# Kernel tuning notes

Hardware: AMD Instinct MI355X
Metric: run time of the kernel (lower is better)

Reference implementation:

```python
import jax, jax.numpy as jnp
from jax import lax
import numpy as np

BALANCE = 1.0  # polynomial kernel: (conv(x,w)+b + BALANCE)**POWER
POWER = 2


def _conv(x, w, b, stride, pad):
    y = lax.conv_general_dilated(
        x, w, window_strides=(stride, stride),
        padding=[(pad, pad), (pad, pad)],
        dimension_numbers=('NCHW', 'OIHW', 'NCHW'))
    return y + b[None, :, None, None]


def kerv2d(x, w, b, stride, pad):
    # PolyKervNets degree-2 polynomial kervolution
    y = _conv(x, w, b, stride, pad) + BALANCE
    return y * y  # (.)**2


def avgpool3s2(x):
    s = lax.reduce_window(x, 0.0, lax.add, (1, 1, 3, 3), (1, 1, 2, 2), 'VALID')
    return s * (1.0 / 9.0)


def setup_inputs() -> dict:
    key = jax.random.key(0)
    ks = jax.random.split(key, 17)
    sc = 0.01  # small init so repeated squaring stays numerically sane
    d = {}
    d['x'] = jax.random.normal(ks[0], (64, 3, 227, 227), jnp.float32)
    d['w1'] = jax.random.normal(ks[1], (96, 3, 11, 11), jnp.float32) * sc
    d['b1'] = jnp.zeros((96,), jnp.float32)
    d['w2'] = jax.random.normal(ks[2], (256, 96, 5, 5), jnp.float32) * sc
    d['b2'] = jnp.zeros((256,), jnp.float32)
    d['w3'] = jax.random.normal(ks[3], (384, 256, 3, 3), jnp.float32) * sc
    d['b3'] = jnp.zeros((384,), jnp.float32)
    d['w4'] = jax.random.normal(ks[4], (384, 384, 3, 3), jnp.float32) * sc
    d['b4'] = jnp.zeros((384,), jnp.float32)
    d['w5'] = jax.random.normal(ks[5], (256, 384, 3, 3), jnp.float32) * sc
    d['b5'] = jnp.zeros((256,), jnp.float32)
    d['fw1'] = jax.random.normal(ks[6], (9216, 4096), jnp.float32) * sc
    d['fb1'] = jnp.zeros((4096,), jnp.float32)
    d['fw2'] = jax.random.normal(ks[7], (4096, 4096), jnp.float32) * sc
    d['fb2'] = jnp.zeros((4096,), jnp.float32)
    d['fw3'] = jax.random.normal(ks[8], (4096, 1000), jnp.float32) * sc
    d['fb3'] = jnp.zeros((1000,), jnp.float32)
    return d


def reference(x, w1, b1, w2, b2, w3, b3, w4, b4, w5, b5,
              fw1, fb1, fw2, fb2, fw3, fb3):
    x = kerv2d(x, w1, b1, stride=4, pad=0)   # [B,96,55,55]
    x = avgpool3s2(x)                        # [B,96,27,27]
    x = kerv2d(x, w2, b2, stride=1, pad=2)   # [B,256,27,27]
    x = avgpool3s2(x)                        # [B,256,13,13]
    x = kerv2d(x, w3, b3, stride=1, pad=1)   # [B,384,13,13]
    x = kerv2d(x, w4, b4, stride=1, pad=1)   # [B,384,13,13]
    x = kerv2d(x, w5, b5, stride=1, pad=1)   # [B,256,13,13]
    x = avgpool3s2(x)                        # [B,256,6,6]
    x = x.reshape(x.shape[0], -1)            # [B,9216]
    x = x @ fw1 + fb1
    x = x @ fw2 + fb2
    x = x @ fw3 + fb3
    return x
```

## Files before the change

### kernel.cpp

```cpp
#include <hip/hip_runtime.h>


typedef _Float16 f16;
typedef _Float16 f16x8 __attribute__((ext_vector_type(8)));
typedef float    f32x4 __attribute__((ext_vector_type(4)));

#define CDIV(a,b) (((a)+(b)-1)/(b))

template<int C,int H,int W,int OC,int R,int S,int PAD,int STRIDE,int OH,int OW,
         bool SCALARB,int BM,int BN>
__global__ __launch_bounds__(256)
void conv_mfma(const f16* __restrict__ in, const f16* __restrict__ wt,
               const float* __restrict__ bias, f16* __restrict__ out)
{
    constexpr int KTOT = C * R * S;
    constexpr int KP   = (KTOT + 31) & ~31;
    constexpr int OHW  = OH * OW;
    constexpr int NTOT = 64 * OHW;
    constexpr int AM   = BM / 32;
    constexpr int AN   = BN / 32;
    constexpr int AU   = BM * 4 / 256;
    constexpr int BU   = BN * 4 / 256;

    __shared__ __align__(16) f16 As[BM * 32];
    __shared__ __align__(16) f16 Bs[BN * 32];

    const int t   = threadIdx.x;
    const int n0  = blockIdx.x * BN;
    const int oc0 = blockIdx.y * BM;

    int a_row[AU], a_g[AU], a_lds[AU]; bool a_ok[AU];
    #pragma unroll
    for (int i = 0; i < AU; ++i) {
        const int u = t + i * 256;
        a_row[i] = u >> 2;
        a_g[i]   = u & 3;
        a_lds[i] = a_row[i] * 32 + ((a_g[i] ^ (a_row[i] & 3)) * 8);
        a_ok[i]  = (oc0 + a_row[i]) < OC;
    }
    int b_row[BU], b_g[BU], b_lds[BU], b_img[BU], b_oy[BU], b_ox[BU]; bool b_ok[BU];
    #pragma unroll
    for (int i = 0; i < BU; ++i) {
        const int u = t + i * 256;
        b_row[i] = u >> 2;
        b_g[i]   = u & 3;
        b_lds[i] = b_row[i] * 32 + ((b_g[i] ^ (b_row[i] & 3)) * 8);
        const int n   = n0 + b_row[i];
        b_ok[i]       = n < NTOT;
        const int ncl = b_ok[i] ? n : 0;
        b_img[i] = ncl / OHW;
        const int rem = ncl - b_img[i] * OHW;
        b_oy[i]  = rem / OW;
        b_ox[i]  = rem - b_oy[i] * OW;
    }

    const int wv = t >> 6;
    const int wm = (wv >> 1) * (BM / 2);
    const int wn = (wv & 1) * (BN / 2);
    const int l  = t & 63;
    const int il = l & 15;
    const int q  = l >> 4;

    f32x4 acc[AM][AN];
    #pragma unroll
    for (int i = 0; i < AM; ++i)
        #pragma unroll
        for (int j = 0; j < AN; ++j)
            acc[i][j] = (f32x4){0.f, 0.f, 0.f, 0.f};

    int4 aReg[AU], bReg[BU];

    auto loadA = [&](int kc) {
        #pragma unroll
        for (int i = 0; i < AU; ++i) {
            int4 v = {0, 0, 0, 0};
            if (a_ok[i])
                v = *(const int4*)(wt + (size_t)(oc0 + a_row[i]) * KP + kc + a_g[i] * 8);
            aReg[i] = v;
        }
    };
    auto loadB = [&](int kc) {
        #pragma unroll
        for (int i = 0; i < BU; ++i) {
            if (SCALARB) {
                const size_t sb = ((size_t)(b_img[i] * H + b_oy[i] * STRIDE) * W
                                   + b_ox[i] * STRIDE) * C;
                union { f16 h[8]; int4 v; } cv;
                #pragma unroll
                for (int j = 0; j < 8; ++j) {
                    const int k = kc + b_g[i] * 8 + j;
                    f16 v = (f16)0.f;
                    if (b_ok[i] && k < KTOT) {
                        const int r  = k / (S * C);
                        const int sc = k - r * (S * C);
                        v = in[sb + (size_t)r * (W * C) + sc];
                    }
                    cv.h[j] = v;
                }
                bReg[i] = cv.v;
            } else {
                const int k8 = kc + b_g[i] * 8;
                const int rs = k8 / C;
                const int c0 = k8 - rs * C;
                const int r  = rs / S;
                const int s  = rs - r * S;
                const int iy = b_oy[i] * STRIDE + r - PAD;
                const int ix = b_ox[i] * STRIDE + s - PAD;
                int4 v = {0, 0, 0, 0};
                if (b_ok[i] && iy >= 0 && iy < H && ix >= 0 && ix < W)
                    v = *(const int4*)(in + ((size_t)(b_img[i] * H + iy) * W + ix) * C + c0);
                bReg[i] = v;
            }
        }
    };

    loadA(0); loadB(0);

    for (int kc = 0; kc < KP; kc += 32) {
        #pragma unroll
        for (int i = 0; i < AU; ++i) *(int4*)&As[a_lds[i]] = aReg[i];
        #pragma unroll
        for (int i = 0; i < BU; ++i) *(int4*)&Bs[b_lds[i]] = bReg[i];
        __syncthreads();

        if (kc + 32 < KP) { loadA(kc + 32); loadB(kc + 32); }

        f16x8 af[AM], bf[AN];
        #pragma unroll
        for (int mi = 0; mi < AM; ++mi) {
            const int row = wm + mi * 16 + il;
            af[mi] = *(const f16x8*)&As[row * 32 + ((q ^ (row & 3)) * 8)];
        }
        #pragma unroll
        for (int ni = 0; ni < AN; ++ni) {
            const int row = wn + ni * 16 + il;
            bf[ni] = *(const f16x8*)&Bs[row * 32 + ((q ^ (row & 3)) * 8)];
        }
        #pragma unroll
        for (int mi = 0; mi < AM; ++mi)
            #pragma unroll
            for (int ni = 0; ni < AN; ++ni)
                acc[mi][ni] = __builtin_amdgcn_mfma_f32_16x16x32_f16(
                    af[mi], bf[ni], acc[mi][ni], 0, 0, 0);
        __syncthreads();
    }

    #pragma unroll
    for (int mi = 0; mi < AM; ++mi) {
        const int ocb = oc0 + wm + mi * 16 + q * 4;
        if (ocb >= OC) continue;
        const float4 bb = *(const float4*)(bias + ocb);
        const float b4[4] = {bb.x + 1.f, bb.y + 1.f, bb.z + 1.f, bb.w + 1.f};
        #pragma unroll
        for (int ni = 0; ni < AN; ++ni) {
            const int nn = n0 + wn + ni * 16 + il;
            if (nn >= NTOT) continue;
            const f32x4 v = acc[mi][ni];
            union { f16 h[4]; uint2 u; } cv;
            const float vv[4] = {v.x, v.y, v.z, v.w};
            #pragma unroll
            for (int rr = 0; rr < 4; ++rr) {
                const float y = vv[rr] + b4[rr];
                cv.h[rr] = (f16)(y * y);
            }
            *(uint2*)(out + (size_t)nn * OC + ocb) = cv.u;
        }
    }
}

template<bool TAIL>
__global__ __launch_bounds__(256)
void fc_mfma2(const f16* __restrict__ X, const float* __restrict__ Wm,
              float* __restrict__ P, int N, int Npad, int K, int kchunk)
{
    __shared__ __align__(16) f16 Xs[64 * 32];
    __shared__ __align__(16) f16 Ws[256 * 32];

    const int t  = threadIdx.x;
    const int n0 = blockIdx.x * 256;
    const int s  = blockIdx.y;
    const int k0 = s * kchunk;
    const int nIter = kchunk / 32;

    const bool wok = !TAIL || (n0 + t) < N;
    const float* __restrict__ wbase = Wm + (size_t)k0 * N + n0 + t;
    const int xm = t >> 2;
    const int xg = t & 3;
    const f16* __restrict__ xbase = X + (size_t)xm * K + k0 + xg * 8;
    const int xoff = xm * 32 + (xg ^ (xm & 3)) * 8;

    const int wq = t >> 6;
    const int l  = t & 63;
    const int il = l & 15;
    const int q  = l >> 4;

    f32x4 acc[4][4];
    #pragma unroll
    for (int i = 0; i < 4; ++i)
        #pragma unroll
        for (int j = 0; j < 4; ++j)
            acc[i][j] = (f32x4){0.f, 0.f, 0.f, 0.f};

    float wreg[4][8];
    int4  xreg;

    auto loadChunk = [&](int it) {
        const size_t kbase = (size_t)it * 32;
        #pragma unroll
        for (int g = 0; g < 4; ++g)
            #pragma unroll
            for (int j = 0; j < 8; ++j)
                wreg[g][j] = wok ? wbase[(kbase + g * 8 + j) * N] : 0.f;
        xreg = *(const int4*)(xbase + kbase);
    };

    loadChunk(0);

    for (int it = 0; it < nIter; ++it) {
        #pragma unroll
        for (int g = 0; g < 4; ++g) {
            f16x8 h;
            #pragma unroll
            for (int j = 0; j < 8; ++j) h[j] = (f16)wreg[g][j];
            *(f16x8*)&Ws[t * 32 + (g ^ (t & 3)) * 8] = h;
        }
        *(int4*)&Xs[xoff] = xreg;
        __syncthreads();

        if (it + 1 < nIter) loadChunk(it + 1);

        f16x8 af[4], bf[4];
        #pragma unroll
        for (int mi = 0; mi < 4; ++mi) {
            const int m = mi * 16 + il;
            af[mi] = *(const f16x8*)&Xs[m * 32 + (q ^ (m & 3)) * 8];
        }
        #pragma unroll
        for (int ni = 0; ni < 4; ++ni) {
            const int n = wq * 64 + ni * 16 + il;
            bf[ni] = *(const f16x8*)&Ws[n * 32 + (q ^ (n & 3)) * 8];
        }
        #pragma unroll
        for (int mi = 0; mi < 4; ++mi)
            #pragma unroll
            for (int ni = 0; ni < 4; ++ni)
                acc[mi][ni] = __builtin_amdgcn_mfma_f32_16x16x32_f16(
                    af[mi], bf[ni], acc[mi][ni], 0, 0, 0);
        __syncthreads();
    }

    float* __restrict__ pb = P + (size_t)s * 64 * Npad + n0;
    #pragma unroll
    for (int mi = 0; mi < 4; ++mi) {
        const int m = mi * 16 + q * 4;
        #pragma unroll
        for (int ni = 0; ni < 4; ++ni) {
            const int n = wq * 64 + ni * 16 + il;
            const f32x4 v = acc[mi][ni];
            const float vv[4] = {v.x, v.y, v.z, v.w};
            #pragma unroll
            for (int rr = 0; rr < 4; ++rr)
                pb[(size_t)(m + rr) * Npad + n] = vv[rr];
        }
    }
}

template<bool F16OUT>
__global__ __launch_bounds__(256)
void fc_reduce(const float* __restrict__ P, const float* __restrict__ bias,
               f16* __restrict__ o16, float* __restrict__ o32,
               int N, int Npad, int S)
{
    const int idx = blockIdx.x * 256 + threadIdx.x;
    const int total = 64 * (N / 4);
    if (idx >= total) return;
    const int n4 = (idx % (N / 4)) * 4;
    const int m  = idx / (N / 4);
    float4 a = *(const float4*)(bias + n4);
    const float* __restrict__ p = P + (size_t)m * Npad + n4;
    for (int s = 0; s < S; ++s) {
        const float4 v = *(const float4*)(p + (size_t)s * 64 * Npad);
        a.x += v.x; a.y += v.y; a.z += v.z; a.w += v.w;
    }
    if (F16OUT) {
        union { f16 h[4]; uint2 u; } cv;
        cv.h[0] = (f16)a.x; cv.h[1] = (f16)a.y;
        cv.h[2] = (f16)a.z; cv.h[3] = (f16)a.w;
        *(uint2*)(o16 + (size_t)m * N + n4) = cv.u;
    } else {
        *(float4*)(o32 + (size_t)m * N + n4) = a;
    }
}

__global__ __launch_bounds__(256)
void avgpool_nhwc(const f16* __restrict__ in, f16* __restrict__ out,
                  int C, int H, int W, int OH, int OW, int total)
{
    const int idx = blockIdx.x * 256 + threadIdx.x;
    if (idx >= total) return;
    const int c   = idx % C;
    int rest      = idx / C;
    const int ox  = rest % OW; rest /= OW;
    const int oy  = rest % OH;
    const int b   = rest / OH;
    const f16* __restrict__ p = in + ((size_t)(b * H + oy * 2) * W + ox * 2) * C + c;
    float s = 0.f;
    #pragma unroll
    for (int r = 0; r < 3; ++r)
        #pragma unroll
        for (int cc = 0; cc < 3; ++cc)
            s += (float)p[(r * W + cc) * C];
    out[idx] = (f16)(s * (1.f / 9.f));
}

__global__ __launch_bounds__(256)
void pool5_ncflat(const f16* __restrict__ in, f16* __restrict__ out)
{
    const int idx = blockIdx.x * 256 + threadIdx.x;
    if (idx >= 64 * 6 * 6 * 256) return;
    const int c  = idx & 255;
    int rest     = idx >> 8;
    const int ox = rest % 6; rest /= 6;
    const int oy = rest % 6;
    const int b  = rest / 6;
    const f16* __restrict__ p = in + ((size_t)(b * 13 + oy * 2) * 13 + ox * 2) * 256 + c;
    float s = 0.f;
    #pragma unroll
    for (int r = 0; r < 3; ++r)
        #pragma unroll
        for (int cc = 0; cc < 3; ++cc)
            s += (float)p[(r * 13 + cc) * 256];
    out[(size_t)b * 9216 + c * 36 + oy * 6 + ox] = (f16)(s * (1.f / 9.f));
}

__global__ __launch_bounds__(256)
void x_to_nhwc(const float* __restrict__ x, f16* __restrict__ o)
{
    const int idx = blockIdx.x * 256 + threadIdx.x;
    if (idx >= 64 * 227 * 227) return;
    const int hw = idx % (227 * 227);
    const int b  = idx / (227 * 227);
    const size_t plane = 227 * 227;
    const float* __restrict__ p = x + (size_t)b * 3 * plane + hw;
    f16* __restrict__ po = o + (size_t)idx * 3;
    po[0] = (f16)p[0];
    po[1] = (f16)p[plane];
    po[2] = (f16)p[2 * plane];
}

__global__ __launch_bounds__(256)
void wt_tf(const float* __restrict__ w, f16* __restrict__ o,
           int OC, int Cc, int R, int S, int KP)
{
    const int idx = blockIdx.x * 256 + threadIdx.x;
    if (idx >= OC * KP) return;
    const int k  = idx % KP;
    const int oc = idx / KP;
    f16 v = (f16)0.f;
    if (k < Cc * R * S) {
        const int rs = k / Cc;
        const int c  = k - rs * Cc;
        const int r  = rs / S;
        const int s  = rs - r * S;
        v = (f16)w[(((size_t)oc * Cc + c) * R + r) * S + s];
    }
    o[idx] = v;
}

extern "C" void kernel_launch(void* const* d_in, const int* in_sizes, int n_in,
                              void* d_out, int out_size, void* d_ws, size_t ws_size,
                              hipStream_t stream)
{
    const float* x   = (const float*)d_in[0];
    const float* w1  = (const float*)d_in[1];
    const float* b1  = (const float*)d_in[2];
    const float* w2  = (const float*)d_in[3];
    const float* b2  = (const float*)d_in[4];
    const float* w3  = (const float*)d_in[5];
    const float* b3  = (const float*)d_in[6];
    const float* w4  = (const float*)d_in[7];
    const float* b4  = (const float*)d_in[8];
    const float* w5  = (const float*)d_in[9];
    const float* b5  = (const float*)d_in[10];
    const float* fw1 = (const float*)d_in[11];
    const float* fb1 = (const float*)d_in[12];
    const float* fw2 = (const float*)d_in[13];
    const float* fb2 = (const float*)d_in[14];
    const float* fw3 = (const float*)d_in[15];
    const float* fb3 = (const float*)d_in[16];
    float* out = (float*)d_out;

    char* ws = (char*)d_ws;
    const size_t MiB = 1024 * 1024;

    f16*   X0  = (f16*)(ws);
    f16*   Xh1 = (f16*)(ws);
    f16*   Xh2 = (f16*)(ws + 2 * MiB);
    f16*   Xh3 = (f16*)(ws + 2 * MiB + 512 * 1024);
    float* P   = (float*)(ws + 3 * MiB);
    f16*   A   = (f16*)(ws + 20 * MiB);
    f16*   Bp  = (f16*)(ws + 58 * MiB);
    f16*   Wt1 = (f16*)(ws + 84 * MiB);
    f16*   Wt2 = Wt1 + (size_t)96  * 384;
    f16*   Wt3 = Wt2 + (size_t)256 * 2400;
    f16*   Wt4 = Wt3 + (size_t)384 * 2304;
    f16*   Wt5 = Wt4 + (size_t)384 * 3456;

    wt_tf<<<CDIV(96  * 384 , 256), 256, 0, stream>>>(w1, Wt1, 96 , 3  , 11, 11, 384);
    wt_tf<<<CDIV(256 * 2400, 256), 256, 0, stream>>>(w2, Wt2, 256, 96 , 5 , 5 , 2400);
    wt_tf<<<CDIV(384 * 2304, 256), 256, 0, stream>>>(w3, Wt3, 384, 256, 3 , 3 , 2304);
    wt_tf<<<CDIV(384 * 3456, 256), 256, 0, stream>>>(w4, Wt4, 384, 384, 3 , 3 , 3456);
    wt_tf<<<CDIV(256 * 3456, 256), 256, 0, stream>>>(w5, Wt5, 256, 384, 3 , 3 , 3456);

    x_to_nhwc<<<CDIV(64 * 227 * 227, 256), 256, 0, stream>>>(x, X0);

    conv_mfma<3,227,227,96,11,11,0,4,55,55,true,128,128>
        <<<dim3(CDIV(64 * 55 * 55, 128), 1), 256, 0, stream>>>(X0, Wt1, b1, A);
    {
        int total = 64 * 27 * 27 * 96;
        avgpool_nhwc<<<CDIV(total, 256), 256, 0, stream>>>(A, Bp, 96, 55, 55, 27, 27, total);
    }
    conv_mfma<96,27,27,256,5,5,2,1,27,27,false,128,128>
        <<<dim3(CDIV(64 * 27 * 27, 128), 2), 256, 0, stream>>>(Bp, Wt2, b2, A);
    {
        int total = 64 * 13 * 13 * 256;
        avgpool_nhwc<<<CDIV(total, 256), 256, 0, stream>>>(A, Bp, 256, 27, 27, 13, 13, total);
    }
    conv_mfma<256,13,13,384,3,3,1,1,13,13,false,128,64>
        <<<dim3(169, 3), 256, 0, stream>>>(Bp, Wt3, b3, A);
    conv_mfma<384,13,13,384,3,3,1,1,13,13,false,128,64>
        <<<dim3(169, 3), 256, 0, stream>>>(A, Wt4, b4, Bp);
    conv_mfma<384,13,13,256,3,3,1,1,13,13,false,128,64>
        <<<dim3(169, 2), 256, 0, stream>>>(Bp, Wt5, b5, A);

    pool5_ncflat<<<CDIV(64 * 6 * 6 * 256, 256), 256, 0, stream>>>(A, Xh1);

    fc_mfma2<false><<<dim3(16, 16), 256, 0, stream>>>(Xh1, fw1, P, 4096, 4096, 9216, 576);
    fc_reduce<true><<<CDIV(64 * 4096 / 4, 256), 256, 0, stream>>>(P, fb1, Xh2, nullptr, 4096, 4096, 16);
    fc_mfma2<false><<<dim3(16, 16), 256, 0, stream>>>(Xh2, fw2, P, 4096, 4096, 4096, 256);
    fc_reduce<true><<<CDIV(64 * 4096 / 4, 256), 256, 0, stream>>>(P, fb2, Xh3, nullptr, 4096, 4096, 16);
    fc_mfma2<true><<<dim3(4, 64), 256, 0, stream>>>(Xh3, fw3, P, 1000, 1024, 4096, 64);
    fc_reduce<false><<<CDIV(64 * 1000 / 4, 256), 256, 0, stream>>>(P, fb3, nullptr, out, 1000, 1024, 64);
}
```

Baseline: 718.9 us.

## Pad conv1 input to 4 channels for vectorized im2col and vectorize avgpool

Pads the input image to NHWC with 4 channels so each conv1 kernel row becomes a contiguous run of 48 halves (12 pixels by 4 channels). The B-tile gather can then use two 8-byte loads instead of eight scalar loads with index math, and the conv1 weights are repacked to match the padded layout. Average pooling is vectorized to process 8 channels per thread with 16-byte loads and stores. The LDS swizzle is changed to use row bits 2-3, and the workspace layout is reshuffled. The cost is a larger padded K for conv1 (544 vs 384), which adds MFMA work that is partly zeros.

```diff
diff --git a/kernel.cpp b/kernel.cpp
--- a/kernel.cpp
+++ b/kernel.cpp
@@ -6,14 +6,15 @@
 typedef float    f32x4 __attribute__((ext_vector_type(4)));
 
 #define CDIV(a,b) (((a)+(b)-1)/(b))
+#define SWZ(row,g) ((g) ^ (((row) >> 2) & 3))
 
 template<int C,int H,int W,int OC,int R,int S,int PAD,int STRIDE,int OH,int OW,
-         bool SCALARB,int BM,int BN>
+         int KRUN,int BM,int BN>
 __global__ __launch_bounds__(256)
 void conv_mfma(const f16* __restrict__ in, const f16* __restrict__ wt,
                const float* __restrict__ bias, f16* __restrict__ out)
 {
-    constexpr int KTOT = C * R * S;
+    constexpr int KTOT = (KRUN > 0) ? (R * KRUN) : (C * R * S);
     constexpr int KP   = (KTOT + 31) & ~31;
     constexpr int OHW  = OH * OW;
     constexpr int NTOT = 64 * OHW;
@@ -35,7 +36,7 @@
         const int u = t + i * 256;
         a_row[i] = u >> 2;
         a_g[i]   = u & 3;
-        a_lds[i] = a_row[i] * 32 + ((a_g[i] ^ (a_row[i] & 3)) * 8);
+        a_lds[i] = a_row[i] * 32 + SWZ(a_row[i], a_g[i]) * 8;
         a_ok[i]  = (oc0 + a_row[i]) < OC;
     }
     int b_row[BU], b_g[BU], b_lds[BU], b_img[BU], b_oy[BU], b_ox[BU]; bool b_ok[BU];
@@ -44,7 +45,7 @@
         const int u = t + i * 256;
         b_row[i] = u >> 2;
         b_g[i]   = u & 3;
-        b_lds[i] = b_row[i] * 32 + ((b_g[i] ^ (b_row[i] & 3)) * 8);
+        b_lds[i] = b_row[i] * 32 + SWZ(b_row[i], b_g[i]) * 8;
         const int n   = n0 + b_row[i];
         b_ok[i]       = n < NTOT;
         const int ncl = b_ok[i] ? n : 0;
@@ -82,22 +83,19 @@
     auto loadB = [&](int kc) {
         #pragma unroll
         for (int i = 0; i < BU; ++i) {
-            if (SCALARB) {
-                const size_t sb = ((size_t)(b_img[i] * H + b_oy[i] * STRIDE) * W
-                                   + b_ox[i] * STRIDE) * C;
-                union { f16 h[8]; int4 v; } cv;
-                #pragma unroll
-                for (int j = 0; j < 8; ++j) {
-                    const int k = kc + b_g[i] * 8 + j;
-                    f16 v = (f16)0.f;
-                    if (b_ok[i] && k < KTOT) {
-                        const int r  = k / (S * C);
-                        const int sc = k - r * (S * C);
-                        v = in[sb + (size_t)r * (W * C) + sc];
-                    }
-                    cv.h[j] = v;
+            if constexpr (KRUN > 0) {
+                const int k8 = kc + b_g[i] * 8;
+                const int r  = k8 / KRUN;
+                const int j0 = k8 - r * KRUN;
+                int4 v = {0, 0, 0, 0};
+                if (b_ok[i] && k8 < KTOT) {
+                    const f16* p = in + ((size_t)(b_img[i] * H + b_oy[i] * STRIDE + r) * W
+                                         + b_ox[i] * STRIDE) * C + j0;
+                    const int2 lo = *(const int2*)p;
+                    const int2 hi = *(const int2*)(p + 4);
+                    v.x = lo.x; v.y = lo.y; v.z = hi.x; v.w = hi.y;
                 }
-                bReg[i] = cv.v;
+                bReg[i] = v;
             } else {
                 const int k8 = kc + b_g[i] * 8;
                 const int rs = k8 / C;
@@ -129,12 +127,12 @@
         #pragma unroll
         for (int mi = 0; mi < AM; ++mi) {
             const int row = wm + mi * 16 + il;
-            af[mi] = *(const f16x8*)&As[row * 32 + ((q ^ (row & 3)) * 8)];
+            af[mi] = *(const f16x8*)&As[row * 32 + SWZ(row, q) * 8];
         }
         #pragma unroll
         for (int ni = 0; ni < AN; ++ni) {
             const int row = wn + ni * 16 + il;
-            bf[ni] = *(const f16x8*)&Bs[row * 32 + ((q ^ (row & 3)) * 8)];
+            bf[ni] = *(const f16x8*)&Bs[row * 32 + SWZ(row, q) * 8];
         }
         #pragma unroll
         for (int mi = 0; mi < AM; ++mi)
@@ -187,7 +185,7 @@
     const int xm = t >> 2;
     const int xg = t & 3;
     const f16* __restrict__ xbase = X + (size_t)xm * K + k0 + xg * 8;
-    const int xoff = xm * 32 + (xg ^ (xm & 3)) * 8;
+    const int xoff = xm * 32 + SWZ(xm, xg) * 8;
 
     const int wq = t >> 6;
     const int l  = t & 63;
@@ -222,7 +220,7 @@
             f16x8 h;
             #pragma unroll
             for (int j = 0; j < 8; ++j) h[j] = (f16)wreg[g][j];
-            *(f16x8*)&Ws[t * 32 + (g ^ (t & 3)) * 8] = h;
+            *(f16x8*)&Ws[t * 32 + SWZ(t, g) * 8] = h;
         }
         *(int4*)&Xs[xoff] = xreg;
         __syncthreads();
@@ -233,12 +231,12 @@
         #pragma unroll
         for (int mi = 0; mi < 4; ++mi) {
             const int m = mi * 16 + il;
-            af[mi] = *(const f16x8*)&Xs[m * 32 + (q ^ (m & 3)) * 8];
+            af[mi] = *(const f16x8*)&Xs[m * 32 + SWZ(m, q) * 8];
         }
         #pragma unroll
         for (int ni = 0; ni < 4; ++ni) {
             const int n = wq * 64 + ni * 16 + il;
-            bf[ni] = *(const f16x8*)&Ws[n * 32 + (q ^ (n & 3)) * 8];
+            bf[ni] = *(const f16x8*)&Ws[n * 32 + SWZ(n, q) * 8];
         }
         #pragma unroll
         for (int mi = 0; mi < 4; ++mi)
@@ -293,24 +291,30 @@
 }
 
 __global__ __launch_bounds__(256)
-void avgpool_nhwc(const f16* __restrict__ in, f16* __restrict__ out,
-                  int C, int H, int W, int OH, int OW, int total)
-{
-    const int idx = blockIdx.x * 256 + threadIdx.x;
-    if (idx >= total) return;
-    const int c   = idx % C;
-    int rest      = idx / C;
+void avgpool_nhwc8(const f16* __restrict__ in, f16* __restrict__ out,
+                   int C8, int C, int H, int W, int OH, int OW, int total8)
+{
+    const int idx = blockIdx.x * 256 + threadIdx.x;
+    if (idx >= total8) return;
+    const int c8  = (idx % C8) * 8;
+    int rest      = idx / C8;
     const int ox  = rest % OW; rest /= OW;
     const int oy  = rest % OH;
     const int b   = rest / OH;
-    const f16* __restrict__ p = in + ((size_t)(b * H + oy * 2) * W + ox * 2) * C + c;
-    float s = 0.f;
+    const f16* __restrict__ p = in + ((size_t)(b * H + oy * 2) * W + ox * 2) * C + c8;
+    float s[8] = {0.f, 0.f, 0.f, 0.f, 0.f, 0.f, 0.f, 0.f};
     #pragma unroll
     for (int r = 0; r < 3; ++r)
         #pragma unroll
-        for (int cc = 0; cc < 3; ++cc)
-            s += (float)p[(r * W + cc) * C];
-    out[idx] = (f16)(s * (1.f / 9.f));
+        for (int cc = 0; cc < 3; ++cc) {
+            const f16x8 v = *(const f16x8*)&p[(r * W + cc) * C];
+            #pragma unroll
+            for (int j = 0; j < 8; ++j) s[j] += (float)v[j];
+        }
+    f16x8 o8;
+    #pragma unroll
+    for (int j = 0; j < 8; ++j) o8[j] = (f16)(s[j] * (1.f / 9.f));
+    *(f16x8*)(out + (size_t)idx * 8) = o8;
 }
 
 __global__ __launch_bounds__(256)
@@ -334,7 +338,7 @@
 }
 
 __global__ __launch_bounds__(256)
-void x_to_nhwc(const float* __restrict__ x, f16* __restrict__ o)
+void x_to_nhwc4(const float* __restrict__ x, f16* __restrict__ o)
 {
     const int idx = blockIdx.x * 256 + threadIdx.x;
     if (idx >= 64 * 227 * 227) return;
@@ -342,10 +346,31 @@
     const int b  = idx / (227 * 227);
     const size_t plane = 227 * 227;
     const float* __restrict__ p = x + (size_t)b * 3 * plane + hw;
-    f16* __restrict__ po = o + (size_t)idx * 3;
-    po[0] = (f16)p[0];
-    po[1] = (f16)p[plane];
-    po[2] = (f16)p[2 * plane];
+    union { f16 h[4]; int2 v; } u;
+    u.h[0] = (f16)p[0];
+    u.h[1] = (f16)p[plane];
+    u.h[2] = (f16)p[2 * plane];
+    u.h[3] = (f16)0.f;
+    *(int2*)(o + (size_t)idx * 4) = u.v;
+}
+
+__global__ __launch_bounds__(256)
+void wt_tf1(const float* __restrict__ w, f16* __restrict__ o)
+{
+    const int idx = blockIdx.x * 256 + threadIdx.x;
+    if (idx >= 96 * 544) return;
+    const int k  = idx % 544;
+    const int oc = idx / 544;
+    f16 v = (f16)0.f;
+    if (k < 528) {
+        const int r   = k / 48;
+        const int rem = k - r * 48;
+        const int s   = rem >> 2;
+        const int c   = rem & 3;
+        if (s < 11 && c < 3)
+            v = (f16)w[(((size_t)oc * 3 + c) * 11 + r) * 11 + s];
+    }
+    o[idx] = v;
 }
 
 __global__ __launch_bounds__(256)
@@ -394,43 +419,43 @@
     const size_t MiB = 1024 * 1024;
 
     f16*   X0  = (f16*)(ws);
-    f16*   Xh1 = (f16*)(ws);
-    f16*   Xh2 = (f16*)(ws + 2 * MiB);
-    f16*   Xh3 = (f16*)(ws + 2 * MiB + 512 * 1024);
-    float* P   = (float*)(ws + 3 * MiB);
-    f16*   A   = (f16*)(ws + 20 * MiB);
-    f16*   Bp  = (f16*)(ws + 58 * MiB);
-    f16*   Wt1 = (f16*)(ws + 84 * MiB);
-    f16*   Wt2 = Wt1 + (size_t)96  * 384;
+    float* P   = (float*)(ws);
+    f16*   Xh1 = (f16*)(ws + 17 * MiB);
+    f16*   Xh2 = (f16*)(ws + 19 * MiB);
+    f16*   Xh3 = (f16*)(ws + 20 * MiB);
+    f16*   A   = (f16*)(ws + 26 * MiB);
+    f16*   Bp  = (f16*)(ws + 62 * MiB);
+    f16*   Wt1 = (f16*)(ws + 72 * MiB);
+    f16*   Wt2 = Wt1 + (size_t)96  * 544;
     f16*   Wt3 = Wt2 + (size_t)256 * 2400;
     f16*   Wt4 = Wt3 + (size_t)384 * 2304;
     f16*   Wt5 = Wt4 + (size_t)384 * 3456;
 
-    wt_tf<<<CDIV(96  * 384 , 256), 256, 0, stream>>>(w1, Wt1, 96 , 3  , 11, 11, 384);
-    wt_tf<<<CDIV(256 * 2400, 256), 256, 0, stream>>>(w2, Wt2, 256, 96 , 5 , 5 , 2400);
-    wt_tf<<<CDIV(384 * 2304, 256), 256, 0, stream>>>(w3, Wt3, 384, 256, 3 , 3 , 2304);
-    wt_tf<<<CDIV(384 * 3456, 256), 256, 0, stream>>>(w4, Wt4, 384, 384, 3 , 3 , 3456);
-    wt_tf<<<CDIV(256 * 3456, 256), 256, 0, stream>>>(w5, Wt5, 256, 384, 3 , 3 , 3456);
-
-    x_to_nhwc<<<CDIV(64 * 227 * 227, 256), 256, 0, stream>>>(x, X0);
-
-    conv_mfma<3,227,227,96,11,11,0,4,55,55,true,128,128>
+    wt_tf1<<<CDIV(96 * 544, 256), 256, 0, stream>>>(w1, Wt1);
+    wt_tf<<<CDIV(256 * 2400, 256), 256, 0, stream>>>(w2, Wt2, 256, 96 , 5, 5, 2400);
+    wt_tf<<<CDIV(384 * 2304, 256), 256, 0, stream>>>(w3, Wt3, 384, 256, 3, 3, 2304);
+    wt_tf<<<CDIV(384 * 3456, 256), 256, 0, stream>>>(w4, Wt4, 384, 384, 3, 3, 3456);
+    wt_tf<<<CDIV(256 * 3456, 256), 256, 0, stream>>>(w5, Wt5, 256, 384, 3, 3, 3456);
+
+    x_to_nhwc4<<<CDIV(64 * 227 * 227, 256), 256, 0, stream>>>(x, X0);
+
+    conv_mfma<4,227,227,96,11,11,0,4,55,55,48,128,128>
         <<<dim3(CDIV(64 * 55 * 55, 128), 1), 256, 0, stream>>>(X0, Wt1, b1, A);
     {
-        int total = 64 * 27 * 27 * 96;
-        avgpool_nhwc<<<CDIV(total, 256), 256, 0, stream>>>(A, Bp, 96, 55, 55, 27, 27, total);
-    }
-    conv_mfma<96,27,27,256,5,5,2,1,27,27,false,128,128>
+        const int total8 = 64 * 27 * 27 * (96 / 8);
+        avgpool_nhwc8<<<CDIV(total8, 256), 256, 0, stream>>>(A, Bp, 96 / 8, 96, 55, 55, 27, 27, total8);
+    }
+    conv_mfma<96,27,27,256,5,5,2,1,27,27,0,128,128>
         <<<dim3(CDIV(64 * 27 * 27, 128), 2), 256, 0, stream>>>(Bp, Wt2, b2, A);
     {
-        int total = 64 * 13 * 13 * 256;
-        avgpool_nhwc<<<CDIV(total, 256), 256, 0, stream>>>(A, Bp, 256, 27, 27, 13, 13, total);
-    }
-    conv_mfma<256,13,13,384,3,3,1,1,13,13,false,128,64>
+        const int total8 = 64 * 13 * 13 * (256 / 8);
+        avgpool_nhwc8<<<CDIV(total8, 256), 256, 0, stream>>>(A, Bp, 256 / 8, 256, 27, 27, 13, 13, total8);
+    }
+    conv_mfma<256,13,13,384,3,3,1,1,13,13,0,128,64>
         <<<dim3(169, 3), 256, 0, stream>>>(Bp, Wt3, b3, A);
-    conv_mfma<384,13,13,384,3,3,1,1,13,13,false,128,64>
+    conv_mfma<384,13,13,384,3,3,1,1,13,13,0,128,64>
         <<<dim3(169, 3), 256, 0, stream>>>(A, Wt4, b4, Bp);
-    conv_mfma<384,13,13,256,3,3,1,1,13,13,false,128,64>
+    conv_mfma<384,13,13,256,3,3,1,1,13,13,0,128,64>
         <<<dim3(169, 2), 256, 0, stream>>>(Bp, Wt5, b5, A);
 
     pool5_ncflat<<<CDIV(64 * 6 * 6 * 256, 256), 256, 0, stream>>>(A, Xh1);
```

Result: faster. 689.7 us (-4.1%).
